# Performance work log

Measured on AMD Instinct MI355X. Metric: run time of the kernel, lower is better.

The kernel has to match this reference:

```python
import jax, jax.numpy as jnp
import numpy as np

EPS = 1e-5        # BatchNorm eps (torch default)
ALPHA = 0.2       # LeakyReLU negative slope


def _gather_nbrs(x, idx):
    # x: (B,N,C), idx: (B,P,S) -> (B,P,S,C)
    B, P, S = idx.shape
    flat = jnp.take_along_axis(x, idx.reshape(B, P * S, 1), axis=1)
    return flat.reshape(B, P, S, x.shape[-1])


def _mlp_layer(x, w, b, g, bt, m, v):
    # 1x1 Conv2d == channel matmul; BN in eval mode with running stats; ReLU.
    h = x @ w.T + b
    h = (h - m) * jax.lax.rsqrt(v + EPS) * g + bt
    return jax.nn.relu(h)


def setup_inputs() -> dict:
    key = jax.random.key(0)
    ks = jax.random.split(key, 8)
    B, N, P, S, C = 16, 4096, 1024, 32, 64
    inp = {
        "xyz": jax.random.normal(ks[0], (B, 3, N), dtype=jnp.float32),
        "points": jax.random.normal(ks[1], (B, C, N), dtype=jnp.float32),
        "fps_idx": jax.random.randint(ks[2], (B, P), 0, N, dtype=jnp.int32),
        "group_idx": jax.random.randint(ks[3], (B, P, S), 0, N, dtype=jnp.int32),
    }
    chans = [(64, 67), (64, 64), (128, 64)]
    for i, (co, ci) in enumerate(chans, start=1):
        kk = jax.random.fold_in(key, 100 + i)
        inp[f"w{i}"] = jax.random.normal(kk, (co, ci), dtype=jnp.float32) * (1.0 / np.sqrt(ci))
        inp[f"b{i}"] = jnp.zeros((co,), jnp.float32)
        inp[f"g{i}"] = jnp.ones((co,), jnp.float32)
        inp[f"beta{i}"] = jnp.zeros((co,), jnp.float32)
        inp[f"m{i}"] = jnp.zeros((co,), jnp.float32)
        inp[f"v{i}"] = jnp.ones((co,), jnp.float32)
    inp["a"] = jax.random.normal(ks[4], (3 + 128, 128), dtype=jnp.float32) * 0.1
    return inp


def reference(xyz, points, fps_idx, group_idx,
              w1, b1, g1, beta1, m1, v1,
              w2, b2, g2, beta2, m2, v2,
              w3, b3, g3, beta3, m3, v3, a):
    xyz_p = jnp.transpose(xyz, (0, 2, 1))      # (B,N,3)
    pts_p = jnp.transpose(points, (0, 2, 1))   # (B,N,C)

    # sample_and_group with precomputed fps / ball-query indices
    new_xyz = jnp.take_along_axis(xyz_p, fps_idx[:, :, None], axis=1)   # (B,P,3)
    fps_feat = jnp.take_along_axis(pts_p, fps_idx[:, :, None], axis=1)  # (B,P,C)
    grouped_xyz = _gather_nbrs(xyz_p, group_idx) - new_xyz[:, :, None, :]  # relative (B,P,S,3)
    grouped_feat = _gather_nbrs(pts_p, group_idx)                           # (B,P,S,C)

    new_points = jnp.concatenate([grouped_xyz, grouped_feat], axis=-1)  # (B,P,S,3+C)
    fps_points = jnp.concatenate([new_xyz, fps_feat], axis=-1)          # (B,P,3+C)

    layers = [(w1, b1, g1, beta1, m1, v1), (w2, b2, g2, beta2, m2, v2), (w3, b3, g3, beta3, m3, v3)]
    for (w, b, g, bt, m, v) in layers:
        new_points = _mlp_layer(new_points, w, b, g, bt, m, v)
        fps_points = _mlp_layer(fps_points, w, b, g, bt, m, v)

    # GraphAttention: delta features -> leaky-relu scores -> softmax over neighbors -> pool
    delta_p = new_xyz[:, :, None, :] - grouped_xyz        # (B,P,S,3)
    delta_h = fps_points[:, :, None, :] - new_points       # (B,P,S,D)
    e = jnp.concatenate([delta_p, delta_h], axis=-1) @ a   # (B,P,S,D)
    e = jnp.where(e > 0, e, ALPHA * e)
    attn = jax.nn.softmax(e, axis=2)                       # softmax over nsample
    pooled = jnp.sum(attn * new_points, axis=2)            # (B,P,D)

    return jnp.transpose(new_xyz, (0, 2, 1)), jnp.transpose(pooled, (0, 2, 1))
```

## Files before the change

### kernel.cpp

```cpp
#include <hip/hip_runtime.h>
#include <hip/hip_bf16.h>

#define Bn 16
#define Nn 4096
#define Pn 1024
#define Sn 32
#define Cn 64
#define EPSn 1e-5f
#define ALPHAn 0.2f
#define LOG2E 1.44269504088896341f

#define W1O 0
#define W2O 4352
#define W3O 8448
#define AO  16640
#define B1O 33536
#define B2O 33600
#define B3O 33664
#define WSF 33792
__device__ __align__(16) float g_W[WSF];

#define F1F 0
#define F2F 24
#define F3F 40
#define F5F 72
#define NFRAG 152
#define WFU (NFRAG * 512)
__device__ __align__(16) unsigned short g_Wf[WFU];

__device__ __align__(16) float g_pts[Bn * Nn * 68];
__device__ __align__(16) float g_fps[Bn * Pn * 132];

typedef __attribute__((ext_vector_type(8))) short short8;
typedef __attribute__((ext_vector_type(4))) float f32x4;

__device__ __forceinline__ void split2(float v, unsigned short& hu, unsigned short& lu) {
  __hip_bfloat16 h = __float2bfloat16(v);
  float hv = __bfloat162float(h);
  __hip_bfloat16 l = __float2bfloat16(v - hv);
  hu = *(unsigned short*)&h;
  lu = *(unsigned short*)&l;
}
__device__ __forceinline__ unsigned short bfh(float v) {
  __hip_bfloat16 h = __float2bfloat16(v);
  return *(unsigned short*)&h;
}
__device__ __forceinline__ float bf2f(unsigned short u) {
  __hip_bfloat16 h = *(__hip_bfloat16*)&u;
  return __bfloat162float(h);
}

#define MFMA_BF16 __builtin_amdgcn_mfma_f32_16x16x32_bf16
#define TERM3(Ci, Ahh, All, Bh, Bl) \
    Ci = MFMA_BF16(Ahh, Bh, Ci, 0, 0, 0); \
    Ci = MFMA_BF16(Ahh, Bl, Ci, 0, 0, 0); \
    Ci = MFMA_BF16(All, Bh, Ci, 0, 0, 0);

__global__ __launch_bounds__(256) void prep_kernel(
    const float* __restrict__ xyz, const float* __restrict__ points,
    const float* __restrict__ w1, const float* __restrict__ b1,
    const float* __restrict__ g1, const float* __restrict__ bt1,
    const float* __restrict__ m1, const float* __restrict__ v1,
    const float* __restrict__ w2, const float* __restrict__ b2,
    const float* __restrict__ g2, const float* __restrict__ bt2,
    const float* __restrict__ m2, const float* __restrict__ v2,
    const float* __restrict__ w3, const float* __restrict__ b3,
    const float* __restrict__ g3, const float* __restrict__ bt3,
    const float* __restrict__ m3, const float* __restrict__ v3,
    const float* __restrict__ a)
{
  if (blockIdx.x < 1024) {
    __shared__ float T[68 * 65];
    const int t = threadIdx.x;
    const int b = blockIdx.x >> 6, n0 = (blockIdx.x & 63) << 6;
    const int nn = t & 63, cgrp = t >> 6;
    #pragma unroll
    for (int k = 0; k < 16; ++k) {
      const int c = cgrp * 16 + k;
      T[c * 65 + nn] = points[(b * Cn + c) * Nn + n0 + nn];
    }
    if (cgrp == 0) {
      #pragma unroll
      for (int d = 0; d < 3; ++d)
        T[(64 + d) * 65 + nn] = xyz[(b * 3 + d) * Nn + n0 + nn];
      T[67 * 65 + nn] = 0.f;
    }
    __syncthreads();
    const int row = t >> 2, part = t & 3;
    float* dst = g_pts + (((long)b << 12) + n0 + row) * 68 + part * 16;
    #pragma unroll
    for (int j = 0; j < 4; ++j) {
      const int o = part * 16 + j * 4;
      float4 v = { T[(o + 0) * 65 + row], T[(o + 1) * 65 + row],
                   T[(o + 2) * 65 + row], T[(o + 3) * 65 + row] };
      *(float4*)(dst + j * 4) = v;
    }
    if (part == 3) {
      float4 v = { T[64 * 65 + row], T[65 * 65 + row],
                   T[66 * 65 + row], T[67 * 65 + row] };
      *(float4*)(dst + 16) = v;
    }
    return;
  }
  const int idx = (blockIdx.x - 1024) * blockDim.x + threadIdx.x;
  if (idx < WSF) {
    float val;
    if (idx < W2O) {
      const int k = idx >> 6, o = idx & 63;
      const float sc = g1[o] * rsqrtf(v1[o] + EPSn);
      val = (k < 64) ? w1[o * 67 + 3 + k] * sc
          : (k < 67) ? w1[o * 67 + (k - 64)] * sc : 0.f;
    } else if (idx < W3O) {
      const int r = idx - W2O, k = r >> 6, o = r & 63;
      val = w2[o * 64 + k] * (g2[o] * rsqrtf(v2[o] + EPSn));
    } else if (idx < AO) {
      const int r = idx - W3O, k = r >> 7, o = r & 127;
      val = w3[o * 64 + k] * (g3[o] * rsqrtf(v3[o] + EPSn));
    } else if (idx < B1O) {
      int r = idx - AO;
      const int half = r / 8448; r -= half * 8448;
      const int k = r >> 6, o = half * 64 + (r & 63);
      val = (k < 128) ? a[(3 + k) * 128 + o]
          : (k < 131) ? a[(k - 128) * 128 + o] : 0.f;
    } else if (idx < B2O) {
      const int o = idx - B1O;
      val = (b1[o] - m1[o]) * (g1[o] * rsqrtf(v1[o] + EPSn)) + bt1[o];
    } else if (idx < B3O) {
      const int o = idx - B2O;
      val = (b2[o] - m2[o]) * (g2[o] * rsqrtf(v2[o] + EPSn)) + bt2[o];
    } else {
      const int o = idx - B3O;
      val = (b3[o] - m3[o]) * (g3[o] * rsqrtf(v3[o] + EPSn)) + bt3[o];
    }
    g_W[idx] = val;
  } else if (idx < WSF + WFU) {
    const int i = idx - WSF;
    const int frag = i >> 9, r = i & 511;
    const int lane = r >> 3, j = r & 7;
    const int quad = lane >> 4, nn = lane & 15;
    int plane, n, k;
    float w;
    if (frag < F2F) {
      const int f = frag;
      plane = f & 1;
      const int c = (f >> 1) & 1, kcch = f >> 2, kc = kcch % 3, ch = kcch / 3;
      n = ch * 32 + c * 16 + nn; k = kc * 32 + quad * 8 + j;
      const float s = g1[n] * rsqrtf(v1[n] + EPSn);
      w = (k < 64) ? w1[n * 67 + 3 + k] * s
        : (k < 67) ? w1[n * 67 + (k - 64)] * s : 0.f;
    } else if (frag < F3F) {
      const int f = frag - F2F;
      plane = f & 1;
      const int c = (f >> 1) & 1, kc = (f >> 2) & 1, ch = f >> 3;
      n = ch * 32 + c * 16 + nn; k = kc * 32 + quad * 8 + j;
      w = w2[n * 64 + k] * (g2[n] * rsqrtf(v2[n] + EPSn));
    } else if (frag < F5F) {
      const int f = frag - F3F;
      plane = f & 1;
      const int c = (f >> 1) & 3, kc = (f >> 3) & 1, ch = f >> 4;
      n = ch * 64 + c * 16 + nn; k = kc * 32 + quad * 8 + j;
      w = w3[n * 64 + k] * (g3[n] * rsqrtf(v3[n] + EPSn));
    } else {
      const int f = frag - F5F;
      plane = f & 1;
      const int c = (f >> 1) & 3, kcch = f >> 3, kc = kcch % 5, ch = kcch / 5;
      n = ch * 64 + c * 16 + nn; k = kc * 32 + quad * 8 + j;
      w = ((k < 128) ? a[(3 + k) * 128 + n]
        : (k < 131) ? a[(k - 128) * 128 + n] : 0.f) * LOG2E;
    }
    unsigned short hu, lu; split2(w, hu, lu);
    g_Wf[i] = plane ? lu : hu;
  }
}

#define XAs 88
#define XHs 152

__global__ __launch_bounds__(256) void fps_kernel(
    const int* __restrict__ fps_idx, float* __restrict__ out)
{
  __shared__ __align__(16) unsigned char LB[15376];
  unsigned short* XAh = (unsigned short*)(LB + 0);
  unsigned short* XAl = (unsigned short*)(LB + 2816);
  unsigned short* XHh = (unsigned short*)(LB + 5632);
  unsigned short* XHl = (unsigned short*)(LB + 10496);
  unsigned short* ZS  = (unsigned short*)(LB + 15360);

  const int t = threadIdx.x, lane = t & 63, w = t >> 6;
  const int quad = lane >> 4, nn = lane & 15;
  const int ch = w >> 1, cl = w & 1;
  const int blk = ((blockIdx.x & 7) << 7) | (blockIdx.x >> 3);
  const int g0 = blk * 16;

  if (t < 4) ((float*)ZS)[t] = 0.f;

  if (t < 128) {
    const int s0 = t >> 3, cg = t & 7;
    const int gp = g0 + s0, b = gp >> 10, p = gp & 1023;
    const int fi = fps_idx[gp];
    const float* frow = g_pts + (((long)b << 12) + fi) * 68;
    const int c0 = cg * 8;
    const float4 va = *(const float4*)(frow + c0);
    const float4 vb = *(const float4*)(frow + c0 + 4);
    short8 hv, lv;
    unsigned short hu, lu;
    split2(va.x, hu, lu); hv[0] = (short)hu; lv[0] = (short)lu;
    split2(va.y, hu, lu); hv[1] = (short)hu; lv[1] = (short)lu;
    split2(va.z, hu, lu); hv[2] = (short)hu; lv[2] = (short)lu;
    split2(va.w, hu, lu); hv[3] = (short)hu; lv[3] = (short)lu;
    split2(vb.x, hu, lu); hv[4] = (short)hu; lv[4] = (short)lu;
    split2(vb.y, hu, lu); hv[5] = (short)hu; lv[5] = (short)lu;
    split2(vb.z, hu, lu); hv[6] = (short)hu; lv[6] = (short)lu;
    split2(vb.w, hu, lu); hv[7] = (short)hu; lv[7] = (short)lu;
    *(short8*)(XAh + s0 * XAs + c0) = hv;
    *(short8*)(XAl + s0 * XAs + c0) = lv;
    if (cg == 0) {
      #pragma unroll
      for (int d = 0; d < 3; ++d) {
        const float v = frow[64 + d];
        unsigned short h2, l2; split2(v, h2, l2);
        XAh[s0 * XAs + 64 + d] = h2; XAl[s0 * XAs + 64 + d] = l2;
        XHh[s0 * XHs + 128 + d] = h2; XHl[s0 * XHs + 128 + d] = l2;
        out[(b * 3 + d) * Pn + p] = v;
        g_fps[(long)gp * 132 + 128 + d] = v;
      }
    } else if (cg == 1) {
      #pragma unroll
      for (int j = 0; j < 13; ++j) { XAh[s0 * XAs + 67 + j] = 0; XAl[s0 * XAs + 67 + j] = 0; }
    } else if (cg == 2) {
      #pragma unroll
      for (int j = 0; j < 13; ++j) { XHh[s0 * XHs + 131 + j] = 0; XHl[s0 * XHs + 131 + j] = 0; }
    }
  }
  __syncthreads();

  f32x4 C[2];
  const int col1 = w * 16 + nn;

  {
    const float bb = g_W[B1O + col1];
    C[0] = (f32x4){bb, bb, bb, bb};
  }
  #pragma unroll
  for (int kc = 0; kc < 3; ++kc) {
    const int ka = kc * 32 + quad * 8;
    const short8 A0h = (ka < 80) ? *(const short8*)(XAh + nn * XAs + ka) : *(const short8*)ZS;
    const short8 A0l = (ka < 80) ? *(const short8*)(XAl + nn * XAs + ka) : *(const short8*)ZS;
    const unsigned short* pf = g_Wf + (((ch * 3 + kc) * 2 + cl) * 2) * 512 + lane * 8;
    const short8 Bh = *(const short8*)pf, Bl = *(const short8*)(pf + 512);
    TERM3(C[0], A0h, A0l, Bh, Bl);
  }
  #pragma unroll
  for (int r = 0; r < 4; ++r) {
    const float v = fmaxf(C[0][r], 0.f);
    unsigned short hu, lu; split2(v, hu, lu);
    XHh[(quad * 4 + r) * XHs + col1] = hu;
    XHl[(quad * 4 + r) * XHs + col1] = lu;
  }
  __syncthreads();

  {
    const float bb = g_W[B2O + col1];
    C[0] = (f32x4){bb, bb, bb, bb};
  }
  #pragma unroll
  for (int kc = 0; kc < 2; ++kc) {
    const int ka = kc * 32 + quad * 8;
    const short8 A0h = *(const short8*)(XHh + nn * XHs + ka);
    const short8 A0l = *(const short8*)(XHl + nn * XHs + ka);
    const unsigned short* pf = g_Wf + (F2F + ((ch * 2 + kc) * 2 + cl) * 2) * 512 + lane * 8;
    const short8 Bh = *(const short8*)pf, Bl = *(const short8*)(pf + 512);
    TERM3(C[0], A0h, A0l, Bh, Bl);
  }
  __syncthreads();
  #pragma unroll
  for (int r = 0; r < 4; ++r) {
    const float v = fmaxf(C[0][r], 0.f);
    unsigned short hu, lu; split2(v, hu, lu);
    XAh[(quad * 4 + r) * XAs + col1] = hu;
    XAl[(quad * 4 + r) * XAs + col1] = lu;
  }
  __syncthreads();

  {
    const float b0 = g_W[B3O + w * 32 + nn];
    const float b1 = g_W[B3O + w * 32 + 16 + nn];
    C[0] = (f32x4){b0, b0, b0, b0};
    C[1] = (f32x4){b1, b1, b1, b1};
  }
  #pragma unroll
  for (int kc = 0; kc < 2; ++kc) {
    const int ka = kc * 32 + quad * 8;
    const short8 A0h = *(const short8*)(XAh + nn * XAs + ka);
    const short8 A0l = *(const short8*)(XAl + nn * XAs + ka);
    #pragma unroll
    for (int c2 = 0; c2 < 2; ++c2) {
      const unsigned short* pf = g_Wf + (F3F + ((ch * 2 + kc) * 4 + cl * 2 + c2) * 2) * 512 + lane * 8;
      const short8 Bh = *(const short8*)pf, Bl = *(const short8*)(pf + 512);
      TERM3(C[c2], A0h, A0l, Bh, Bl);
    }
  }
  __syncthreads();
  #pragma unroll
  for (int c2 = 0; c2 < 2; ++c2) {
    const int col = w * 32 + c2 * 16 + nn;
    #pragma unroll
    for (int r = 0; r < 4; ++r) {
      const float v = fmaxf(C[c2][r], 0.f);
      unsigned short hu, lu; split2(v, hu, lu);
      XHh[(quad * 4 + r) * XHs + col] = hu;
      XHl[(quad * 4 + r) * XHs + col] = lu;
    }
  }
  __syncthreads();

  C[0] = (f32x4){0.f,0.f,0.f,0.f}; C[1] = C[0];
  #pragma unroll
  for (int kc = 0; kc < 5; ++kc) {
    const int ka = kc * 32 + quad * 8;
    const short8 A0h = (ka < 144) ? *(const short8*)(XHh + nn * XHs + ka) : *(const short8*)ZS;
    const short8 A0l = (ka < 144) ? *(const short8*)(XHl + nn * XHs + ka) : *(const short8*)ZS;
    #pragma unroll
    for (int c2 = 0; c2 < 2; ++c2) {
      const unsigned short* pf = g_Wf + (F5F + ((ch * 5 + kc) * 4 + cl * 2 + c2) * 2) * 512 + lane * 8;
      const short8 Bh = *(const short8*)pf, Bl = *(const short8*)(pf + 512);
      TERM3(C[c2], A0h, A0l, Bh, Bl);
    }
  }
  #pragma unroll
  for (int c2 = 0; c2 < 2; ++c2) {
    const int col = w * 32 + c2 * 16 + nn;
    #pragma unroll
    for (int r = 0; r < 4; ++r)
      g_fps[(long)(g0 + quad * 4 + r) * 132 + col] = C[c2][r];
  }
}

#define OXB0 0
#define OXB1 9728
#define OFS  19456
#define OZS  20480
#define LDSB 20496

__global__ __launch_bounds__(256, 7) void fused_kernel(
    const int* __restrict__ group_idx, float* __restrict__ out)
{
  __shared__ __align__(16) unsigned char LB[LDSB];
  unsigned short* const XB0 = (unsigned short*)(LB + OXB0);
  unsigned short* const XB1 = (unsigned short*)(LB + OXB1);
  float*          FS = (float*)(LB + OFS);
  unsigned short* ZS = (unsigned short*)(LB + OZS);

  const int t = threadIdx.x, lane = t & 63, w = t >> 6;
  const int quad = lane >> 4, nn = lane & 15;
  const int ch = w >> 1, cl = w & 1;
  const int blk = ((blockIdx.x & 7) << 10) | (blockIdx.x >> 3);
  const int base = blk * 2;
  const int b = base >> 10, p0 = base & 1023;

  {
    const int gi = t >> 7, cc = t & 127;
    FS[t] = g_fps[(long)(base + gi) * 132 + cc];
  }
  if (t < 4) ((float*)ZS)[t] = 0.f;

  {
    const int s0 = t >> 3, cg = t & 7;
    const int c0 = cg * 8;
    #pragma unroll
    for (int gi = 0; gi < 2; ++gi) {
      unsigned short* XBg = gi ? XB1 : XB0;
      const int gidx = group_idx[(base + gi) * Sn + s0];
      const float* prow = g_pts + (((long)b << 12) + gidx) * 68;
      const float4 va = *(const float4*)(prow + c0);
      const float4 vb = *(const float4*)(prow + c0 + 4);
      unsigned q0, q1, q2, q3;
      asm("v_cvt_pk_bf16_f32 %0, %1, %2" : "=v"(q0) : "v"(va.x), "v"(va.y));
      asm("v_cvt_pk_bf16_f32 %0, %1, %2" : "=v"(q1) : "v"(va.z), "v"(va.w));
      asm("v_cvt_pk_bf16_f32 %0, %1, %2" : "=v"(q2) : "v"(vb.x), "v"(vb.y));
      asm("v_cvt_pk_bf16_f32 %0, %1, %2" : "=v"(q3) : "v"(vb.z), "v"(vb.w));
      uint4 hv = {q0, q1, q2, q3};
      *(uint4*)(XBg + s0 * XHs + c0) = hv;
      if (cg == 0) {
        #pragma unroll
        for (int d = 0; d < 3; ++d) {
          const float r = prow[64 + d] - g_fps[(long)(base + gi) * 132 + 128 + d];
          const unsigned short hu = bfh(r);
          XBg[s0 * XHs + 64 + d] = hu;
          XBg[s0 * XHs + 128 + d] = hu;
        }
      } else if (cg == 1) {
        #pragma unroll
        for (int j = 0; j < 15; ++j) XBg[s0 * XHs + 67 + j] = 0;
      } else if (cg == 2) {
        #pragma unroll
        for (int j = 0; j < 14; ++j) XBg[s0 * XHs + 82 + j] = 0;
      } else if (cg == 3) {
        #pragma unroll
        for (int j = 0; j < 13; ++j) XBg[s0 * XHs + 131 + j] = 0;
      }
    }
  }
  __syncthreads();

  const int col1 = w * 16 + nn;

  {
    f32x4 C00, C01, C10, C11;
    const float bb = g_W[B1O + col1];
    C00 = (f32x4){bb, bb, bb, bb};
    C01 = C00; C10 = C00; C11 = C00;
    #pragma unroll
    for (int kc = 0; kc < 3; ++kc) {
      const int ka = kc * 32 + quad * 8;
      const unsigned short* pf = g_Wf + (((ch * 3 + kc) * 2 + cl) * 2) * 512 + lane * 8;
      const short8 Bh = *(const short8*)pf, Bl = *(const short8*)(pf + 512);
      const short8 A00 = *(const short8*)(XB0 + nn * XHs + ka);
      const short8 A01 = *(const short8*)(XB0 + (16 + nn) * XHs + ka);
      const short8 A10 = *(const short8*)(XB1 + nn * XHs + ka);
      const short8 A11 = *(const short8*)(XB1 + (16 + nn) * XHs + ka);
      C00 = MFMA_BF16(A00, Bh, C00, 0, 0, 0);
      C00 = MFMA_BF16(A00, Bl, C00, 0, 0, 0);
      C01 = MFMA_BF16(A01, Bh, C01, 0, 0, 0);
      C01 = MFMA_BF16(A01, Bl, C01, 0, 0, 0);
      C10 = MFMA_BF16(A10, Bh, C10, 0, 0, 0);
      C10 = MFMA_BF16(A10, Bl, C10, 0, 0, 0);
      C11 = MFMA_BF16(A11, Bh, C11, 0, 0, 0);
      C11 = MFMA_BF16(A11, Bl, C11, 0, 0, 0);
    }
    __syncthreads();
    #pragma unroll
    for (int r = 0; r < 4; ++r) {
      XB0[(quad * 4 + r) * XHs + col1]      = bfh(fmaxf(C00[r], 0.f));
      XB0[(16 + quad * 4 + r) * XHs + col1] = bfh(fmaxf(C01[r], 0.f));
      XB1[(quad * 4 + r) * XHs + col1]      = bfh(fmaxf(C10[r], 0.f));
      XB1[(16 + quad * 4 + r) * XHs + col1] = bfh(fmaxf(C11[r], 0.f));
    }
  }
  __syncthreads();

  {
    f32x4 C00, C01, C10, C11;
    const float bb = g_W[B2O + col1];
    C00 = (f32x4){bb, bb, bb, bb};
    C01 = C00; C10 = C00; C11 = C00;
    #pragma unroll
    for (int kc = 0; kc < 2; ++kc) {
      const int ka = kc * 32 + quad * 8;
      const unsigned short* pf = g_Wf + (F2F + ((ch * 2 + kc) * 2 + cl) * 2) * 512 + lane * 8;
      const short8 Bh = *(const short8*)pf, Bl = *(const short8*)(pf + 512);
      const short8 A00 = *(const short8*)(XB0 + nn * XHs + ka);
      const short8 A01 = *(const short8*)(XB0 + (16 + nn) * XHs + ka);
      const short8 A10 = *(const short8*)(XB1 + nn * XHs + ka);
      const short8 A11 = *(const short8*)(XB1 + (16 + nn) * XHs + ka);
      C00 = MFMA_BF16(A00, Bh, C00, 0, 0, 0);
      C00 = MFMA_BF16(A00, Bl, C00, 0, 0, 0);
      C01 = MFMA_BF16(A01, Bh, C01, 0, 0, 0);
      C01 = MFMA_BF16(A01, Bl, C01, 0, 0, 0);
      C10 = MFMA_BF16(A10, Bh, C10, 0, 0, 0);
      C10 = MFMA_BF16(A10, Bl, C10, 0, 0, 0);
      C11 = MFMA_BF16(A11, Bh, C11, 0, 0, 0);
      C11 = MFMA_BF16(A11, Bl, C11, 0, 0, 0);
    }
    #pragma unroll
    for (int r = 0; r < 4; ++r) {
      XB0[(quad * 4 + r) * XHs + 64 + col1]      = bfh(fmaxf(C00[r], 0.f));
      XB0[(16 + quad * 4 + r) * XHs + 64 + col1] = bfh(fmaxf(C01[r], 0.f));
      XB1[(quad * 4 + r) * XHs + 64 + col1]      = bfh(fmaxf(C10[r], 0.f));
      XB1[(16 + quad * 4 + r) * XHs + 64 + col1] = bfh(fmaxf(C11[r], 0.f));
    }
  }
  __syncthreads();

  {
    f32x4 C0[4], C1[4];
    const float b0 = g_W[B3O + w * 32 + nn];
    const float b1 = g_W[B3O + w * 32 + 16 + nn];
    C0[0] = (f32x4){b0, b0, b0, b0};
    C0[1] = (f32x4){b1, b1, b1, b1};
    C0[2] = C0[0]; C0[3] = C0[1];
    C1[0] = C0[0]; C1[1] = C0[1]; C1[2] = C0[0]; C1[3] = C0[1];
    #pragma unroll
    for (int kc = 0; kc < 2; ++kc) {
      const int ka = 64 + kc * 32 + quad * 8;
      const short8 A00 = *(const short8*)(XB0 + nn * XHs + ka);
      const short8 A01 = *(const short8*)(XB0 + (16 + nn) * XHs + ka);
      const short8 A10 = *(const short8*)(XB1 + nn * XHs + ka);
      const short8 A11 = *(const short8*)(XB1 + (16 + nn) * XHs + ka);
      #pragma unroll
      for (int c2 = 0; c2 < 2; ++c2) {
        const unsigned short* pf = g_Wf + (F3F + ((ch * 2 + kc) * 4 + cl * 2 + c2) * 2) * 512 + lane * 8;
        const short8 Bh = *(const short8*)pf, Bl = *(const short8*)(pf + 512);
        C0[0 + c2] = MFMA_BF16(A00, Bh, C0[0 + c2], 0, 0, 0);
        C0[0 + c2] = MFMA_BF16(A00, Bl, C0[0 + c2], 0, 0, 0);
        C0[2 + c2] = MFMA_BF16(A01, Bh, C0[2 + c2], 0, 0, 0);
        C0[2 + c2] = MFMA_BF16(A01, Bl, C0[2 + c2], 0, 0, 0);
        C1[0 + c2] = MFMA_BF16(A10, Bh, C1[0 + c2], 0, 0, 0);
        C1[0 + c2] = MFMA_BF16(A10, Bl, C1[0 + c2], 0, 0, 0);
        C1[2 + c2] = MFMA_BF16(A11, Bh, C1[2 + c2], 0, 0, 0);
        C1[2 + c2] = MFMA_BF16(A11, Bl, C1[2 + c2], 0, 0, 0);
      }
    }
    __syncthreads();
    #pragma unroll
    for (int c2 = 0; c2 < 2; ++c2) {
      const int col = w * 32 + c2 * 16 + nn;
      #pragma unroll
      for (int r = 0; r < 4; ++r) {
        XB0[(quad * 4 + r) * XHs + col]      = bfh(fmaxf(C0[0 + c2][r], 0.f));
        XB0[(16 + quad * 4 + r) * XHs + col] = bfh(fmaxf(C0[2 + c2][r], 0.f));
        XB1[(quad * 4 + r) * XHs + col]      = bfh(fmaxf(C1[0 + c2][r], 0.f));
        XB1[(16 + quad * 4 + r) * XHs + col] = bfh(fmaxf(C1[2 + c2][r], 0.f));
      }
    }
  }
  __syncthreads();

  f32x4 C0[4], C1[4];
  {
    const float e00 = FS[w * 32 + nn];
    const float e01 = FS[w * 32 + 16 + nn];
    const float e10 = FS[128 + w * 32 + nn];
    const float e11 = FS[128 + w * 32 + 16 + nn];
    C0[0] = (f32x4){-e00, -e00, -e00, -e00};
    C0[1] = (f32x4){-e01, -e01, -e01, -e01};
    C0[2] = C0[0]; C0[3] = C0[1];
    C1[0] = (f32x4){-e10, -e10, -e10, -e10};
    C1[1] = (f32x4){-e11, -e11, -e11, -e11};
    C1[2] = C1[0]; C1[3] = C1[1];
  }
  #pragma unroll
  for (int kc = 0; kc < 5; ++kc) {
    const int ka = kc * 32 + quad * 8;
    const short8 A00 = (ka < 144) ? *(const short8*)(XB0 + nn * XHs + ka) : *(const short8*)ZS;
    const short8 A01 = (ka < 144) ? *(const short8*)(XB0 + (16 + nn) * XHs + ka) : *(const short8*)ZS;
    const short8 A10 = (ka < 144) ? *(const short8*)(XB1 + nn * XHs + ka) : *(const short8*)ZS;
    const short8 A11 = (ka < 144) ? *(const short8*)(XB1 + (16 + nn) * XHs + ka) : *(const short8*)ZS;
    #pragma unroll
    for (int c2 = 0; c2 < 2; ++c2) {
      const unsigned short* pf = g_Wf + (F5F + ((ch * 5 + kc) * 4 + cl * 2 + c2) * 2) * 512 + lane * 8;
      const short8 Bh = *(const short8*)pf, Bl = *(const short8*)(pf + 512);
      C0[0 + c2] = MFMA_BF16(A00, Bh, C0[0 + c2], 0, 0, 0);
      C0[0 + c2] = MFMA_BF16(A00, Bl, C0[0 + c2], 0, 0, 0);
      C0[2 + c2] = MFMA_BF16(A01, Bh, C0[2 + c2], 0, 0, 0);
      C0[2 + c2] = MFMA_BF16(A01, Bl, C0[2 + c2], 0, 0, 0);
      C1[0 + c2] = MFMA_BF16(A10, Bh, C1[0 + c2], 0, 0, 0);
      C1[0 + c2] = MFMA_BF16(A10, Bl, C1[0 + c2], 0, 0, 0);
      C1[2 + c2] = MFMA_BF16(A11, Bh, C1[2 + c2], 0, 0, 0);
      C1[2 + c2] = MFMA_BF16(A11, Bl, C1[2 + c2], 0, 0, 0);
    }
  }

  #pragma unroll
  for (int gi = 0; gi < 2; ++gi) {
    unsigned short* XBg = gi ? XB1 : XB0;
    #pragma unroll
    for (int c2 = 0; c2 < 2; ++c2) {
      const int col = w * 32 + c2 * 16 + nn;
      f32x4* Cg = gi ? C1 : C0;
      float tmin = 3.4e38f;
      #pragma unroll
      for (int mi = 0; mi < 2; ++mi)
        #pragma unroll
        for (int r = 0; r < 4; ++r) {
          const int idx = mi * 2 + c2;
          const float cv = Cg[idx][r];
          const float tv = fminf(cv, 0.2f * cv);
          Cg[idx][r] = tv;
          tmin = fminf(tmin, tv);
        }
      tmin = fminf(tmin, __shfl_xor(tmin, 16));
      tmin = fminf(tmin, __shfl_xor(tmin, 32));
      float den = 0.f, pool = 0.f;
      #pragma unroll
      for (int mi = 0; mi < 2; ++mi)
        #pragma unroll
        for (int r = 0; r < 4; ++r) {
          const int idx = mi * 2 + c2;
          const float wgt = __builtin_amdgcn_exp2f(tmin - Cg[idx][r]);
          den += wgt;
          pool = fmaf(wgt, bf2f(XBg[(mi * 16 + quad * 4 + r) * XHs + col]), pool);
        }
      den  += __shfl_xor(den, 16);  den  += __shfl_xor(den, 32);
      pool += __shfl_xor(pool, 16); pool += __shfl_xor(pool, 32);
      if (quad == 0)
        out[Bn * 3 * Pn + ((b << 7) + col) * Pn + p0 + gi] =
            pool * __builtin_amdgcn_rcpf(den);
    }
  }
}

extern "C" void kernel_launch(void* const* d_in, const int* in_sizes, int n_in,
                              void* d_out, int out_size, void* d_ws, size_t ws_size,
                              hipStream_t stream) {
  const float* xyz       = (const float*)d_in[0];
  const float* points    = (const float*)d_in[1];
  const int*   fps_idx   = (const int*)d_in[2];
  const int*   group_idx = (const int*)d_in[3];

  const int prep_blocks = 1024 + (WSF + WFU + 255) / 256;
  prep_kernel<<<prep_blocks, 256, 0, stream>>>(
      xyz, points,
      (const float*)d_in[4],  (const float*)d_in[5],
      (const float*)d_in[6],  (const float*)d_in[7],
      (const float*)d_in[8],  (const float*)d_in[9],
      (const float*)d_in[10], (const float*)d_in[11],
      (const float*)d_in[12], (const float*)d_in[13],
      (const float*)d_in[14], (const float*)d_in[15],
      (const float*)d_in[16], (const float*)d_in[17],
      (const float*)d_in[18], (const float*)d_in[19],
      (const float*)d_in[20], (const float*)d_in[21],
      (const float*)d_in[22]);

  fps_kernel<<<1024, 256, 0, stream>>>(fps_idx, (float*)d_out);

  fused_kernel<<<Bn * Pn / 2, 256, 0, stream>>>(group_idx, (float*)d_out);
}
```

Measured before the change: 230.9 us.

## Stage pooled output in scratch and transpose it in a separate kernel

The fused kernel now writes pooled results contiguously per point to a scratch buffer instead of doing strided scattered stores into the channel-major output. A new tiled LDS transpose kernel then writes the output with coalesced stores. The fps feature tile is read directly into registers rather than staged through LDS, which frees LDS, and the occupancy hint rises from 7 to 8 blocks. The cost is an extra kernel launch plus a write and re-read of the scratch buffer.

```diff
diff --git a/kernel.cpp b/kernel.cpp
--- a/kernel.cpp
+++ b/kernel.cpp
@@ -30,6 +30,7 @@
 
 __device__ __align__(16) float g_pts[Bn * Nn * 68];
 __device__ __align__(16) float g_fps[Bn * Pn * 132];
+__device__ __align__(16) float g_tmp[Bn * Pn * 128];
 
 typedef __attribute__((ext_vector_type(8))) short short8;
 typedef __attribute__((ext_vector_type(4))) float f32x4;
@@ -336,19 +337,37 @@
   }
 }
 
+__global__ __launch_bounds__(256) void transpose_out(float* __restrict__ out)
+{
+  __shared__ float T[64 * 129];
+  const int t = threadIdx.x;
+  const int b = blockIdx.x >> 4, p0 = (blockIdx.x & 15) << 6;
+  const int c = t & 127, ph = t >> 7;
+  #pragma unroll
+  for (int pp = 0; pp < 32; ++pp) {
+    const int pi = ph * 32 + pp;
+    T[pi * 129 + c] = g_tmp[(((long)b << 10) + p0 + pi) * 128 + c];
+  }
+  __syncthreads();
+  const int pn = t & 63, cg = t >> 6;
+  #pragma unroll
+  for (int k = 0; k < 32; ++k) {
+    const int cc = cg * 32 + k;
+    out[Bn * 3 * Pn + ((b << 7) + cc) * Pn + p0 + pn] = T[pn * 129 + cc];
+  }
+}
+
 #define OXB0 0
 #define OXB1 9728
-#define OFS  19456
-#define OZS  20480
-#define LDSB 20496
-
-__global__ __launch_bounds__(256, 7) void fused_kernel(
-    const int* __restrict__ group_idx, float* __restrict__ out)
+#define OZS  19456
+#define LDSB 19472
+
+__global__ __launch_bounds__(256, 8) void fused_kernel(
+    const int* __restrict__ group_idx)
 {
   __shared__ __align__(16) unsigned char LB[LDSB];
   unsigned short* const XB0 = (unsigned short*)(LB + OXB0);
   unsigned short* const XB1 = (unsigned short*)(LB + OXB1);
-  float*          FS = (float*)(LB + OFS);
   unsigned short* ZS = (unsigned short*)(LB + OZS);
 
   const int t = threadIdx.x, lane = t & 63, w = t >> 6;
@@ -356,12 +375,13 @@
   const int ch = w >> 1, cl = w & 1;
   const int blk = ((blockIdx.x & 7) << 10) | (blockIdx.x >> 3);
   const int base = blk * 2;
-  const int b = base >> 10, p0 = base & 1023;
-
-  {
-    const int gi = t >> 7, cc = t & 127;
-    FS[t] = g_fps[(long)(base + gi) * 132 + cc];
-  }
+  const int b = base >> 10;
+
+  const float e00 = g_fps[(long)base * 132 + w * 32 + nn];
+  const float e01 = g_fps[(long)base * 132 + w * 32 + 16 + nn];
+  const float e10 = g_fps[(long)(base + 1) * 132 + w * 32 + nn];
+  const float e11 = g_fps[(long)(base + 1) * 132 + w * 32 + 16 + nn];
+
   if (t < 4) ((float*)ZS)[t] = 0.f;
 
   {
@@ -518,10 +538,6 @@
 
   f32x4 C0[4], C1[4];
   {
-    const float e00 = FS[w * 32 + nn];
-    const float e01 = FS[w * 32 + 16 + nn];
-    const float e10 = FS[128 + w * 32 + nn];
-    const float e11 = FS[128 + w * 32 + 16 + nn];
     C0[0] = (f32x4){-e00, -e00, -e00, -e00};
     C0[1] = (f32x4){-e01, -e01, -e01, -e01};
     C0[2] = C0[0]; C0[3] = C0[1];
@@ -584,7 +600,7 @@
       den  += __shfl_xor(den, 16);  den  += __shfl_xor(den, 32);
       pool += __shfl_xor(pool, 16); pool += __shfl_xor(pool, 32);
       if (quad == 0)
-        out[Bn * 3 * Pn + ((b << 7) + col) * Pn + p0 + gi] =
+        g_tmp[(long)(base + gi) * 128 + col] =
             pool * __builtin_amdgcn_rcpf(den);
     }
   }
@@ -614,5 +630,7 @@
 
   fps_kernel<<<1024, 256, 0, stream>>>(fps_idx, (float*)d_out);
 
-  fused_kernel<<<Bn * Pn / 2, 256, 0, stream>>>(group_idx, (float*)d_out);
-}
+  fused_kernel<<<Bn * Pn / 2, 256, 0, stream>>>(group_idx);
+
+  transpose_out<<<Bn * 16, 256, 0, stream>>>((float*)d_out);
+}
```

After: 298.8 us. 29.4% more time.
